# Kernel tuning notes

Measured on AMD Instinct MI355X. Metric: run time of the kernel, lower is better.

Reference implementation:

```python
import jax, jax.numpy as jnp
import numpy as np

E = 512
H = 8
HD = E // H  # head dim = 64


def setup_inputs() -> dict:
    key = jax.random.key(0)
    ks = jax.random.split(key, 7)
    B, P, R = 32, 4096, 64
    visual_tokens = jax.random.normal(ks[0], (B, P, E), dtype=jnp.float32)
    region_tokens = jax.random.normal(ks[1], (B, R, E), dtype=jnp.float32)
    distance_mask = jax.random.uniform(ks[2], (B, P, R), dtype=jnp.float32)
    s = 1.0 / np.sqrt(E)
    in_proj_weight = jax.random.uniform(ks[3], (3 * E, E), jnp.float32, -s, s)
    in_proj_bias = jnp.zeros((3 * E,), jnp.float32)
    out_proj_weight = jax.random.uniform(ks[4], (E, E), jnp.float32, -s, s)
    out_proj_bias = jnp.zeros((E,), jnp.float32)
    return {
        "visual_tokens": visual_tokens,
        "region_tokens": region_tokens,
        "distance_mask": distance_mask,
        "in_proj_weight": in_proj_weight,
        "in_proj_bias": in_proj_bias,
        "out_proj_weight": out_proj_weight,
        "out_proj_bias": out_proj_bias,
    }


def reference(visual_tokens, region_tokens, distance_mask,
              in_proj_weight, in_proj_bias, out_proj_weight, out_proj_bias):
    B, P, _ = visual_tokens.shape
    R = region_tokens.shape[1]
    # additive logit bias derived from distance mask (broadcast over heads,
    # instead of repeating B*H copies like the torch code)
    bias = (1.0 - distance_mask.astype(jnp.float32)) * -1e9  # [B,P,R]
    Wq, Wk, Wv = in_proj_weight[:E], in_proj_weight[E:2 * E], in_proj_weight[2 * E:]
    bq, bk, bv = in_proj_bias[:E], in_proj_bias[E:2 * E], in_proj_bias[2 * E:]
    v32 = visual_tokens.astype(jnp.float32)
    r32 = region_tokens.astype(jnp.float32)
    q = (v32 @ Wq.T + bq).reshape(B, P, H, HD)
    k = (r32 @ Wk.T + bk).reshape(B, R, H, HD)
    v = (r32 @ Wv.T + bv).reshape(B, R, H, HD)
    scale = 1.0 / jnp.sqrt(jnp.float32(HD))
    scores = jnp.einsum('bphd,brhd->bhpr', q, k) * scale + bias[:, None]  # [B,H,P,R]
    attn = jax.nn.softmax(scores, axis=-1)
    ctx = jnp.einsum('bhpr,brhd->bphd', attn, v).reshape(B, P, E)
    attended = ctx @ out_proj_weight.T + out_proj_bias
    return attended.astype(visual_tokens.dtype) + visual_tokens
```

## Files before the change

### kernel.cpp

```cpp
#include <hip/hip_runtime.h>
#include <hip/hip_bf16.h>

typedef unsigned short u16;
typedef unsigned int u32;

using bf16x8 = __attribute__((ext_vector_type(8))) short;
using f32x4  = __attribute__((ext_vector_type(4))) float;

#define MFMA16(a, b, c) __builtin_amdgcn_mfma_f32_16x16x32_bf16((a), (b), (c), 0, 0, 0)

__device__ __forceinline__ u16 f2bf(float f) {
    u32 u = __builtin_bit_cast(u32, f);
    u = (u + 0x7fffu + ((u >> 16) & 1u)) >> 16;
    return (u16)u;
}

__global__ __launch_bounds__(256, 2) void frgca_prep(
    const float* __restrict__ region,
    const float* __restrict__ in_w,
    const float* __restrict__ in_b,
    const float* __restrict__ out_w,
    u16* __restrict__ wq, u16* __restrict__ wo,
    u16* __restrict__ kt, u16* __restrict__ vt)
{
    __shared__ u16 As2[64 * 520];
    const int tid = threadIdx.x;
    const int bid = blockIdx.x;

    if (bid < 32) {
        const float4* w4q = (const float4*)in_w;
        const float4* w4o = (const float4*)out_w;
        int t = bid * 256 + tid;
#pragma unroll
        for (int i = 0; i < 16; ++i) {
            int idx = t + i * 8192;
            float4 v;
            u16* dst;
            if (idx < 65536) { v = w4q[idx]; dst = wq + idx * 4; }
            else             { v = w4o[idx - 65536]; dst = wo + (idx - 65536) * 4; }
            ushort4 o;
            o.x = f2bf(v.x); o.y = f2bf(v.y); o.z = f2bf(v.z); o.w = f2bf(v.w);
            *(ushort4*)dst = o;
        }
        return;
    }

    const int t2 = bid - 32;
    const int b  = t2 >> 2;
    const int nc = t2 & 3;

    {
        const float4* r4 = (const float4*)(region + (size_t)b * 64 * 512);
#pragma unroll
        for (int i = 0; i < 32; ++i) {
            int f4  = tid + i * 256;
            int row = f4 >> 7;
            int c4  = f4 & 127;
            float4 v = r4[f4];
            ushort4 o;
            o.x = f2bf(v.x); o.y = f2bf(v.y); o.z = f2bf(v.z); o.w = f2bf(v.w);
            *(ushort4*)&As2[row * 520 + c4 * 4] = o;
        }
    }
    __syncthreads();

    const int lane = tid & 63, w = tid >> 6;
    const int lo16 = lane & 15, g = lane >> 4;
    const int e0 = nc * 256 + w * 64;

    f32x4 acc[4][4];
#pragma unroll
    for (int mt = 0; mt < 4; ++mt)
#pragma unroll
        for (int nt = 0; nt < 4; ++nt)
            acc[mt][nt] = f32x4{0.f, 0.f, 0.f, 0.f};

    const float* w2 = in_w + 512 * 512;

#pragma unroll 2
    for (int ks = 0; ks < 16; ++ks) {
        const int kc = ks * 32 + 8 * g;
        bf16x8 a[4], bb[4];
#pragma unroll
        for (int mt = 0; mt < 4; ++mt)
            a[mt] = *(const bf16x8*)&As2[(mt * 16 + lo16) * 520 + kc];
#pragma unroll
        for (int nt = 0; nt < 4; ++nt) {
            const int e = e0 + nt * 16 + lo16;
            const float* src = w2 + (size_t)e * 512 + kc;
            float4 v0 = *(const float4*)src;
            float4 v1 = *(const float4*)(src + 4);
            bf16x8 bv;
            bv[0] = (short)f2bf(v0.x); bv[1] = (short)f2bf(v0.y);
            bv[2] = (short)f2bf(v0.z); bv[3] = (short)f2bf(v0.w);
            bv[4] = (short)f2bf(v1.x); bv[5] = (short)f2bf(v1.y);
            bv[6] = (short)f2bf(v1.z); bv[7] = (short)f2bf(v1.w);
            bb[nt] = bv;
        }
#pragma unroll
        for (int mt = 0; mt < 4; ++mt)
#pragma unroll
            for (int nt = 0; nt < 4; ++nt)
                acc[mt][nt] = MFMA16(a[mt], bb[nt], acc[mt][nt]);
    }

#pragma unroll
    for (int nt = 0; nt < 4; ++nt) {
        const int e = e0 + nt * 16 + lo16;
        const float bias = in_b[512 + e];
#pragma unroll
        for (int mt = 0; mt < 4; ++mt)
#pragma unroll
            for (int i = 0; i < 4; ++i) {
                const int r = mt * 16 + 4 * g + i;
                const u16 o = f2bf(acc[mt][nt][i] + bias);
                if (e < 512) {
                    const int h = e >> 6, d = e & 63;
                    kt[(((size_t)(b * 8 + h)) * 64 + r) * 64 + d] = o;
                } else {
                    const int e2 = e - 512;
                    const int h = e2 >> 6, d = e2 & 63;
                    vt[(((size_t)(b * 8 + h)) * 64 + d) * 64 + r] = o;
                }
            }
    }
}

__global__ __launch_bounds__(512, 2) void frgca_main(
    const float* __restrict__ visual,
    const float* __restrict__ mask,
    const float* __restrict__ in_b,
    const float* __restrict__ out_b,
    const u16* __restrict__ wq, const u16* __restrict__ wo,
    const u16* __restrict__ kt, const u16* __restrict__ vt,
    float* __restrict__ out)
{
    __shared__ char regA[73728];
    __shared__ float Ms[64][65];

    const int tid = threadIdx.x;
    const int w = tid >> 6, lane = tid & 63;
    const int lo16 = lane & 15, g = lane >> 4;
    const int pt = blockIdx.x, b = blockIdx.y;
    const int P0 = pt * 64;
    const size_t vbase = ((size_t)(b * 4096 + P0)) * 512;

    u16* As = (u16*)regA;

    {
        const float4* v4 = (const float4*)(visual + vbase);
#pragma unroll
        for (int i = 0; i < 16; ++i) {
            int f4  = tid + i * 512;
            int row = f4 >> 7, c4 = f4 & 127;
            float4 v = v4[f4];
            ushort4 o;
            o.x = f2bf(v.x); o.y = f2bf(v.y); o.z = f2bf(v.z); o.w = f2bf(v.w);
            *(ushort4*)&As[row * 520 + c4 * 4] = o;
        }
        const float4* m4 = (const float4*)(mask + ((size_t)(b * 4096 + P0)) * 64);
#pragma unroll
        for (int i = 0; i < 2; ++i) {
            int f4  = tid + i * 512;
            int row = f4 >> 4, c4 = f4 & 15;
            float4 v = m4[f4];
            float* dst = &Ms[row][c4 * 4];
            dst[0] = (1.0f - v.x) * -1e9f;
            dst[1] = (1.0f - v.y) * -1e9f;
            dst[2] = (1.0f - v.z) * -1e9f;
            dst[3] = (1.0f - v.w) * -1e9f;
        }
    }
    __syncthreads();

    const int e0 = w * 64;

    f32x4 acc[4][4];
#pragma unroll
    for (int mt = 0; mt < 4; ++mt)
#pragma unroll
        for (int nt = 0; nt < 4; ++nt)
            acc[mt][nt] = f32x4{0.f, 0.f, 0.f, 0.f};

#pragma unroll 2
    for (int ks = 0; ks < 16; ++ks) {
        const int kc = ks * 32 + 8 * g;
        bf16x8 a[4], bb[4];
#pragma unroll
        for (int mt = 0; mt < 4; ++mt)
            a[mt] = *(const bf16x8*)&As[(mt * 16 + lo16) * 520 + kc];
#pragma unroll
        for (int nt = 0; nt < 4; ++nt)
            bb[nt] = *(const bf16x8*)&wq[((size_t)(e0 + nt * 16 + lo16)) * 512 + kc];
#pragma unroll
        for (int mt = 0; mt < 4; ++mt)
#pragma unroll
            for (int nt = 0; nt < 4; ++nt)
                acc[mt][nt] = MFMA16(a[mt], bb[nt], acc[mt][nt]);
    }
#pragma unroll
    for (int nt = 0; nt < 4; ++nt) {
        const float bq = in_b[e0 + nt * 16 + lo16];
#pragma unroll
        for (int mt = 0; mt < 4; ++mt)
#pragma unroll
            for (int i = 0; i < 4; ++i)
                acc[mt][nt][i] += bq;
    }
    __syncthreads();

    u16* Qw = (u16*)(regA + w * 9216);
#pragma unroll
    for (int mt = 0; mt < 4; ++mt)
#pragma unroll
        for (int nt = 0; nt < 4; ++nt)
#pragma unroll
            for (int i = 0; i < 4; ++i)
                Qw[(mt * 16 + 4 * g + i) * 72 + (nt * 16 + lo16)] = f2bf(acc[mt][nt][i]);

    const u16* KtH = kt + ((size_t)(b * 8 + w)) * 64 * 64;
    f32x4 s[4][4];
#pragma unroll
    for (int mt = 0; mt < 4; ++mt)
#pragma unroll
        for (int nt = 0; nt < 4; ++nt)
            s[mt][nt] = f32x4{0.f, 0.f, 0.f, 0.f};

#pragma unroll
    for (int ks = 0; ks < 2; ++ks) {
        const int kc = ks * 32 + 8 * g;
        bf16x8 ak[4], bq_[4];
#pragma unroll
        for (int mt = 0; mt < 4; ++mt)
            ak[mt] = *(const bf16x8*)&KtH[(mt * 16 + lo16) * 64 + kc];
#pragma unroll
        for (int nt = 0; nt < 4; ++nt)
            bq_[nt] = *(const bf16x8*)&Qw[(nt * 16 + lo16) * 72 + kc];
#pragma unroll
        for (int mt = 0; mt < 4; ++mt)
#pragma unroll
            for (int nt = 0; nt < 4; ++nt)
                s[mt][nt] = MFMA16(ak[mt], bq_[nt], s[mt][nt]);
    }

#pragma unroll
    for (int nt = 0; nt < 4; ++nt) {
        const int p = nt * 16 + lo16;
        float mx = -3.4e38f;
#pragma unroll
        for (int mt = 0; mt < 4; ++mt)
#pragma unroll
            for (int i = 0; i < 4; ++i) {
                float v = s[mt][nt][i] * 0.125f + Ms[p][mt * 16 + 4 * g + i];
                s[mt][nt][i] = v;
                mx = fmaxf(mx, v);
            }
        mx = fmaxf(mx, __shfl_xor(mx, 16));
        mx = fmaxf(mx, __shfl_xor(mx, 32));
        float sum = 0.f;
#pragma unroll
        for (int mt = 0; mt < 4; ++mt)
#pragma unroll
            for (int i = 0; i < 4; ++i) {
                float ev = __expf(s[mt][nt][i] - mx);
                s[mt][nt][i] = ev;
                sum += ev;
            }
        sum += __shfl_xor(sum, 16);
        sum += __shfl_xor(sum, 32);
        const float inv = 1.0f / sum;
#pragma unroll
        for (int mt = 0; mt < 4; ++mt)
#pragma unroll
            for (int i = 0; i < 4; ++i)
                Qw[p * 72 + (mt * 16 + 4 * g + i)] = f2bf(s[mt][nt][i] * inv);
    }

    const u16* VtH = vt + ((size_t)(b * 8 + w)) * 64 * 64;
    f32x4 c_[4][4];
#pragma unroll
    for (int mt = 0; mt < 4; ++mt)
#pragma unroll
        for (int nt = 0; nt < 4; ++nt)
            c_[mt][nt] = f32x4{0.f, 0.f, 0.f, 0.f};

#pragma unroll
    for (int ks = 0; ks < 2; ++ks) {
        const int kc = ks * 32 + 8 * g;
        bf16x8 av[4], bs_[4];
#pragma unroll
        for (int mt = 0; mt < 4; ++mt)
            av[mt] = *(const bf16x8*)&VtH[(mt * 16 + lo16) * 64 + kc];
#pragma unroll
        for (int nt = 0; nt < 4; ++nt)
            bs_[nt] = *(const bf16x8*)&Qw[(nt * 16 + lo16) * 72 + kc];
#pragma unroll
        for (int mt = 0; mt < 4; ++mt)
#pragma unroll
            for (int nt = 0; nt < 4; ++nt)
                c_[mt][nt] = MFMA16(av[mt], bs_[nt], c_[mt][nt]);
    }
    __syncthreads();

    u16* Cs = (u16*)regA;
#pragma unroll
    for (int mt = 0; mt < 4; ++mt)
#pragma unroll
        for (int nt = 0; nt < 4; ++nt)
#pragma unroll
            for (int i = 0; i < 4; ++i) {
                const int d = mt * 16 + 4 * g + i;
                const int p = nt * 16 + lo16;
                Cs[p * 520 + (w * 64 + d)] = f2bf(c_[mt][nt][i]);
            }
    __syncthreads();

    f32x4 o_[4][4];
#pragma unroll
    for (int mt = 0; mt < 4; ++mt)
#pragma unroll
        for (int nt = 0; nt < 4; ++nt)
            o_[mt][nt] = f32x4{0.f, 0.f, 0.f, 0.f};

#pragma unroll 2
    for (int ks = 0; ks < 16; ++ks) {
        const int kc = ks * 32 + 8 * g;
        bf16x8 a[4], bb[4];
#pragma unroll
        for (int mt = 0; mt < 4; ++mt)
            a[mt] = *(const bf16x8*)&Cs[(mt * 16 + lo16) * 520 + kc];
#pragma unroll
        for (int nt = 0; nt < 4; ++nt)
            bb[nt] = *(const bf16x8*)&wo[((size_t)(e0 + nt * 16 + lo16)) * 512 + kc];
#pragma unroll
        for (int mt = 0; mt < 4; ++mt)
#pragma unroll
            for (int nt = 0; nt < 4; ++nt)
                o_[mt][nt] = MFMA16(a[mt], bb[nt], o_[mt][nt]);
    }

#pragma unroll
    for (int nt = 0; nt < 4; ++nt) {
        const int e = e0 + nt * 16 + lo16;
        const float bo = out_b[e];
#pragma unroll
        for (int mt = 0; mt < 4; ++mt)
#pragma unroll
            for (int i = 0; i < 4; ++i) {
                const int p = mt * 16 + 4 * g + i;
                const size_t gid = vbase + (size_t)p * 512 + e;
                out[gid] = o_[mt][nt][i] + bo + visual[gid];
            }
    }
}

extern "C" void kernel_launch(void* const* d_in, const int* in_sizes, int n_in,
                              void* d_out, int out_size, void* d_ws, size_t ws_size,
                              hipStream_t stream) {
    const float* visual = (const float*)d_in[0];
    const float* region = (const float*)d_in[1];
    const float* mask   = (const float*)d_in[2];
    const float* in_w   = (const float*)d_in[3];
    const float* in_b   = (const float*)d_in[4];
    const float* out_w  = (const float*)d_in[5];
    const float* out_b  = (const float*)d_in[6];
    float* out = (float*)d_out;

    char* ws = (char*)d_ws;
    u16* wq = (u16*)(ws + 0);
    u16* wo = (u16*)(ws + 524288);
    u16* kt = (u16*)(ws + 1048576);
    u16* vt = (u16*)(ws + 3145728);

    frgca_prep<<<dim3(160), dim3(256), 0, stream>>>(region, in_w, in_b, out_w, wq, wo, kt, vt);
    frgca_main<<<dim3(64, 32), dim3(512), 0, stream>>>(visual, mask, in_b, out_b, wq, wo, kt, vt, out);
}
```

Baseline: 478.1 us.

## Swizzle LDS layouts, prefetch weights, and raise occupancy of fused attention kernel

Replaces padded shared-memory tiles with XOR-swizzled layouts (1024-byte rows for activations, 128-byte rows per wave for Q/probabilities, XOR-indexed mask), which cuts LDS use from about 90KB to 80KB. Launch bounds change from 2 to 4 blocks, and the weight loads in both projection GEMMs are software-pipelined with register double-buffering. K and V fragments are loaded early so their latency is hidden. The aim is fewer bank conflicts and better latency hiding, at the cost of register pressure under the tighter occupancy bound. LDS size may still limit residency below the new bound.

```diff
diff --git a/kernel.cpp b/kernel.cpp
--- a/kernel.cpp
+++ b/kernel.cpp
@@ -126,7 +126,7 @@
     }
 }
 
-__global__ __launch_bounds__(512, 2) void frgca_main(
+__global__ __launch_bounds__(512, 4) void frgca_main(
     const float* __restrict__ visual,
     const float* __restrict__ mask,
     const float* __restrict__ in_b,
@@ -135,17 +135,16 @@
     const u16* __restrict__ kt, const u16* __restrict__ vt,
     float* __restrict__ out)
 {
-    __shared__ char regA[73728];
-    __shared__ float Ms[64][65];
+    __shared__ char regA[65536];
+    __shared__ float Ms[4096];
 
     const int tid = threadIdx.x;
     const int w = tid >> 6, lane = tid & 63;
     const int lo16 = lane & 15, g = lane >> 4;
+    const int xr = (lo16 & 7) << 4;
     const int pt = blockIdx.x, b = blockIdx.y;
     const int P0 = pt * 64;
     const size_t vbase = ((size_t)(b * 4096 + P0)) * 512;
-
-    u16* As = (u16*)regA;
 
     {
         const float4* v4 = (const float4*)(visual + vbase);
@@ -156,19 +155,19 @@
             float4 v = v4[f4];
             ushort4 o;
             o.x = f2bf(v.x); o.y = f2bf(v.y); o.z = f2bf(v.z); o.w = f2bf(v.w);
-            *(ushort4*)&As[row * 520 + c4 * 4] = o;
+            *(ushort4*)(regA + row * 1024 + ((c4 * 8) ^ ((row & 7) << 4))) = o;
         }
         const float4* m4 = (const float4*)(mask + ((size_t)(b * 4096 + P0)) * 64);
 #pragma unroll
         for (int i = 0; i < 2; ++i) {
-            int f4  = tid + i * 512;
-            int row = f4 >> 4, c4 = f4 & 15;
+            int f4 = tid + i * 512;
+            int p = f4 >> 4, r0 = (f4 & 15) * 4;
             float4 v = m4[f4];
-            float* dst = &Ms[row][c4 * 4];
-            dst[0] = (1.0f - v.x) * -1e9f;
-            dst[1] = (1.0f - v.y) * -1e9f;
-            dst[2] = (1.0f - v.z) * -1e9f;
-            dst[3] = (1.0f - v.w) * -1e9f;
+            int pb = p * 64, px = p & 31;
+            Ms[pb + ((r0 + 0) ^ px)] = (1.0f - v.x) * -1e9f;
+            Ms[pb + ((r0 + 1) ^ px)] = (1.0f - v.y) * -1e9f;
+            Ms[pb + ((r0 + 2) ^ px)] = (1.0f - v.z) * -1e9f;
+            Ms[pb + ((r0 + 3) ^ px)] = (1.0f - v.w) * -1e9f;
         }
     }
     __syncthreads();
@@ -182,22 +181,56 @@
         for (int nt = 0; nt < 4; ++nt)
             acc[mt][nt] = f32x4{0.f, 0.f, 0.f, 0.f};
 
-#pragma unroll 2
+    const u16* wqR0 = wq + ((size_t)(e0 + 0 * 16 + lo16)) * 512;
+    const u16* wqR1 = wq + ((size_t)(e0 + 1 * 16 + lo16)) * 512;
+    const u16* wqR2 = wq + ((size_t)(e0 + 2 * 16 + lo16)) * 512;
+    const u16* wqR3 = wq + ((size_t)(e0 + 3 * 16 + lo16)) * 512;
+    bf16x8 nb0 = *(const bf16x8*)&wqR0[8 * g];
+    bf16x8 nb1 = *(const bf16x8*)&wqR1[8 * g];
+    bf16x8 nb2 = *(const bf16x8*)&wqR2[8 * g];
+    bf16x8 nb3 = *(const bf16x8*)&wqR3[8 * g];
+
+#pragma unroll
     for (int ks = 0; ks < 16; ++ks) {
         const int kc = ks * 32 + 8 * g;
-        bf16x8 a[4], bb[4];
-#pragma unroll
-        for (int mt = 0; mt < 4; ++mt)
-            a[mt] = *(const bf16x8*)&As[(mt * 16 + lo16) * 520 + kc];
-#pragma unroll
-        for (int nt = 0; nt < 4; ++nt)
-            bb[nt] = *(const bf16x8*)&wq[((size_t)(e0 + nt * 16 + lo16)) * 512 + kc];
-#pragma unroll
-        for (int mt = 0; mt < 4; ++mt)
-#pragma unroll
-            for (int nt = 0; nt < 4; ++nt)
-                acc[mt][nt] = MFMA16(a[mt], bb[nt], acc[mt][nt]);
-    }
+        bf16x8 cb0 = nb0, cb1 = nb1, cb2 = nb2, cb3 = nb3;
+        if (ks < 15) {
+            const int kn = kc + 32;
+            nb0 = *(const bf16x8*)&wqR0[kn];
+            nb1 = *(const bf16x8*)&wqR1[kn];
+            nb2 = *(const bf16x8*)&wqR2[kn];
+            nb3 = *(const bf16x8*)&wqR3[kn];
+        }
+        bf16x8 a[4];
+#pragma unroll
+        for (int mt = 0; mt < 4; ++mt)
+            a[mt] = *(const bf16x8*)(regA + (mt * 16 + lo16) * 1024 + ((kc * 2) ^ xr));
+        acc[0][0] = MFMA16(a[0], cb0, acc[0][0]);
+        acc[1][0] = MFMA16(a[1], cb0, acc[1][0]);
+        acc[2][0] = MFMA16(a[2], cb0, acc[2][0]);
+        acc[3][0] = MFMA16(a[3], cb0, acc[3][0]);
+        acc[0][1] = MFMA16(a[0], cb1, acc[0][1]);
+        acc[1][1] = MFMA16(a[1], cb1, acc[1][1]);
+        acc[2][1] = MFMA16(a[2], cb1, acc[2][1]);
+        acc[3][1] = MFMA16(a[3], cb1, acc[3][1]);
+        acc[0][2] = MFMA16(a[0], cb2, acc[0][2]);
+        acc[1][2] = MFMA16(a[1], cb2, acc[1][2]);
+        acc[2][2] = MFMA16(a[2], cb2, acc[2][2]);
+        acc[3][2] = MFMA16(a[3], cb2, acc[3][2]);
+        acc[0][3] = MFMA16(a[0], cb3, acc[0][3]);
+        acc[1][3] = MFMA16(a[1], cb3, acc[1][3]);
+        acc[2][3] = MFMA16(a[2], cb3, acc[2][3]);
+        acc[3][3] = MFMA16(a[3], cb3, acc[3][3]);
+    }
+
+    const u16* KtH = kt + ((size_t)(b * 8 + w)) * 4096;
+    bf16x8 ak[4][2];
+#pragma unroll
+    for (int ks2 = 0; ks2 < 2; ++ks2)
+#pragma unroll
+        for (int mt = 0; mt < 4; ++mt)
+            ak[mt][ks2] = *(const bf16x8*)&KtH[(mt * 16 + lo16) * 64 + ks2 * 32 + 8 * g];
+
 #pragma unroll
     for (int nt = 0; nt < 4; ++nt) {
         const float bq = in_b[e0 + nt * 16 + lo16];
@@ -209,16 +242,18 @@
     }
     __syncthreads();
 
-    u16* Qw = (u16*)(regA + w * 9216);
-#pragma unroll
-    for (int mt = 0; mt < 4; ++mt)
-#pragma unroll
-        for (int nt = 0; nt < 4; ++nt)
-#pragma unroll
-            for (int i = 0; i < 4; ++i)
-                Qw[(mt * 16 + 4 * g + i) * 72 + (nt * 16 + lo16)] = f2bf(acc[mt][nt][i]);
-
-    const u16* KtH = kt + ((size_t)(b * 8 + w)) * 64 * 64;
+    char* Qw = regA + w * 8192;
+#pragma unroll
+    for (int mt = 0; mt < 4; ++mt)
+#pragma unroll
+        for (int nt = 0; nt < 4; ++nt)
+#pragma unroll
+            for (int i = 0; i < 4; ++i) {
+                const int p = mt * 16 + 4 * g + i;
+                const int d = nt * 16 + lo16;
+                *(u16*)(Qw + p * 128 + ((d * 2) ^ ((p & 7) << 4))) = f2bf(acc[mt][nt][i]);
+            }
+
     f32x4 s[4][4];
 #pragma unroll
     for (int mt = 0; mt < 4; ++mt)
@@ -227,31 +262,37 @@
             s[mt][nt] = f32x4{0.f, 0.f, 0.f, 0.f};
 
 #pragma unroll
-    for (int ks = 0; ks < 2; ++ks) {
-        const int kc = ks * 32 + 8 * g;
-        bf16x8 ak[4], bq_[4];
-#pragma unroll
-        for (int mt = 0; mt < 4; ++mt)
-            ak[mt] = *(const bf16x8*)&KtH[(mt * 16 + lo16) * 64 + kc];
-#pragma unroll
-        for (int nt = 0; nt < 4; ++nt)
-            bq_[nt] = *(const bf16x8*)&Qw[(nt * 16 + lo16) * 72 + kc];
+    for (int ks2 = 0; ks2 < 2; ++ks2) {
+        const int kcb = (ks2 * 32 + 8 * g) * 2;
+        bf16x8 bq_[4];
+#pragma unroll
+        for (int nt = 0; nt < 4; ++nt)
+            bq_[nt] = *(const bf16x8*)(Qw + (nt * 16 + lo16) * 128 + (kcb ^ xr));
 #pragma unroll
         for (int mt = 0; mt < 4; ++mt)
 #pragma unroll
             for (int nt = 0; nt < 4; ++nt)
-                s[mt][nt] = MFMA16(ak[mt], bq_[nt], s[mt][nt]);
-    }
+                s[mt][nt] = MFMA16(ak[mt][ks2], bq_[nt], s[mt][nt]);
+    }
+
+    const u16* VtH = vt + ((size_t)(b * 8 + w)) * 4096;
+    bf16x8 av[4][2];
+#pragma unroll
+    for (int ks2 = 0; ks2 < 2; ++ks2)
+#pragma unroll
+        for (int mt = 0; mt < 4; ++mt)
+            av[mt][ks2] = *(const bf16x8*)&VtH[(mt * 16 + lo16) * 64 + ks2 * 32 + 8 * g];
 
 #pragma unroll
     for (int nt = 0; nt < 4; ++nt) {
         const int p = nt * 16 + lo16;
+        const int pb = p * 64, px = p & 31;
         float mx = -3.4e38f;
 #pragma unroll
         for (int mt = 0; mt < 4; ++mt)
 #pragma unroll
             for (int i = 0; i < 4; ++i) {
-                float v = s[mt][nt][i] * 0.125f + Ms[p][mt * 16 + 4 * g + i];
+                float v = s[mt][nt][i] * 0.125f + Ms[pb + ((mt * 16 + 4 * g + i) ^ px)];
                 s[mt][nt][i] = v;
                 mx = fmaxf(mx, v);
             }
@@ -272,11 +313,12 @@
 #pragma unroll
         for (int mt = 0; mt < 4; ++mt)
 #pragma unroll
-            for (int i = 0; i < 4; ++i)
-                Qw[p * 72 + (mt * 16 + 4 * g + i)] = f2bf(s[mt][nt][i] * inv);
-    }
-
-    const u16* VtH = vt + ((size_t)(b * 8 + w)) * 64 * 64;
+            for (int i = 0; i < 4; ++i) {
+                const int r = mt * 16 + 4 * g + i;
+                *(u16*)(Qw + p * 128 + ((r * 2) ^ ((p & 7) << 4))) = f2bf(s[mt][nt][i] * inv);
+            }
+    }
+
     f32x4 c_[4][4];
 #pragma unroll
     for (int mt = 0; mt < 4; ++mt)
@@ -285,33 +327,29 @@
             c_[mt][nt] = f32x4{0.f, 0.f, 0.f, 0.f};
 
 #pragma unroll
-    for (int ks = 0; ks < 2; ++ks) {
-        const int kc = ks * 32 + 8 * g;
-        bf16x8 av[4], bs_[4];
-#pragma unroll
-        for (int mt = 0; mt < 4; ++mt)
-            av[mt] = *(const bf16x8*)&VtH[(mt * 16 + lo16) * 64 + kc];
-#pragma unroll
-        for (int nt = 0; nt < 4; ++nt)
-            bs_[nt] = *(const bf16x8*)&Qw[(nt * 16 + lo16) * 72 + kc];
+    for (int ks2 = 0; ks2 < 2; ++ks2) {
+        const int kcb = (ks2 * 32 + 8 * g) * 2;
+        bf16x8 bs_[4];
+#pragma unroll
+        for (int nt = 0; nt < 4; ++nt)
+            bs_[nt] = *(const bf16x8*)(Qw + (nt * 16 + lo16) * 128 + (kcb ^ xr));
 #pragma unroll
         for (int mt = 0; mt < 4; ++mt)
 #pragma unroll
             for (int nt = 0; nt < 4; ++nt)
-                c_[mt][nt] = MFMA16(av[mt], bs_[nt], c_[mt][nt]);
+                c_[mt][nt] = MFMA16(av[mt][ks2], bs_[nt], c_[mt][nt]);
     }
     __syncthreads();
 
-    u16* Cs = (u16*)regA;
-#pragma unroll
-    for (int mt = 0; mt < 4; ++mt)
-#pragma unroll
-        for (int nt = 0; nt < 4; ++nt)
-#pragma unroll
-            for (int i = 0; i < 4; ++i) {
-                const int d = mt * 16 + 4 * g + i;
+#pragma unroll
+    for (int mt = 0; mt < 4; ++mt)
+#pragma unroll
+        for (int nt = 0; nt < 4; ++nt)
+#pragma unroll
+            for (int i = 0; i < 4; ++i) {
                 const int p = nt * 16 + lo16;
-                Cs[p * 520 + (w * 64 + d)] = f2bf(c_[mt][nt][i]);
+                const int c = e0 + mt * 16 + 4 * g + i;
+                *(u16*)(regA + p * 1024 + ((c * 2) ^ ((p & 7) << 4))) = f2bf(c_[mt][nt][i]);
             }
     __syncthreads();
 
@@ -322,21 +360,46 @@
         for (int nt = 0; nt < 4; ++nt)
             o_[mt][nt] = f32x4{0.f, 0.f, 0.f, 0.f};
 
-#pragma unroll 2
+    const u16* woR0 = wo + ((size_t)(e0 + 0 * 16 + lo16)) * 512;
+    const u16* woR1 = wo + ((size_t)(e0 + 1 * 16 + lo16)) * 512;
+    const u16* woR2 = wo + ((size_t)(e0 + 2 * 16 + lo16)) * 512;
+    const u16* woR3 = wo + ((size_t)(e0 + 3 * 16 + lo16)) * 512;
+    bf16x8 ob0 = *(const bf16x8*)&woR0[8 * g];
+    bf16x8 ob1 = *(const bf16x8*)&woR1[8 * g];
+    bf16x8 ob2 = *(const bf16x8*)&woR2[8 * g];
+    bf16x8 ob3 = *(const bf16x8*)&woR3[8 * g];
+
+#pragma unroll
     for (int ks = 0; ks < 16; ++ks) {
         const int kc = ks * 32 + 8 * g;
-        bf16x8 a[4], bb[4];
-#pragma unroll
-        for (int mt = 0; mt < 4; ++mt)
-            a[mt] = *(const bf16x8*)&Cs[(mt * 16 + lo16) * 520 + kc];
-#pragma unroll
-        for (int nt = 0; nt < 4; ++nt)
-            bb[nt] = *(const bf16x8*)&wo[((size_t)(e0 + nt * 16 + lo16)) * 512 + kc];
-#pragma unroll
-        for (int mt = 0; mt < 4; ++mt)
-#pragma unroll
-            for (int nt = 0; nt < 4; ++nt)
-                o_[mt][nt] = MFMA16(a[mt], bb[nt], o_[mt][nt]);
+        bf16x8 cb0 = ob0, cb1 = ob1, cb2 = ob2, cb3 = ob3;
+        if (ks < 15) {
+            const int kn = kc + 32;
+            ob0 = *(const bf16x8*)&woR0[kn];
+            ob1 = *(const bf16x8*)&woR1[kn];
+            ob2 = *(const bf16x8*)&woR2[kn];
+            ob3 = *(const bf16x8*)&woR3[kn];
+        }
+        bf16x8 a[4];
+#pragma unroll
+        for (int mt = 0; mt < 4; ++mt)
+            a[mt] = *(const bf16x8*)(regA + (mt * 16 + lo16) * 1024 + ((kc * 2) ^ xr));
+        o_[0][0] = MFMA16(a[0], cb0, o_[0][0]);
+        o_[1][0] = MFMA16(a[1], cb0, o_[1][0]);
+        o_[2][0] = MFMA16(a[2], cb0, o_[2][0]);
+        o_[3][0] = MFMA16(a[3], cb0, o_[3][0]);
+        o_[0][1] = MFMA16(a[0], cb1, o_[0][1]);
+        o_[1][1] = MFMA16(a[1], cb1, o_[1][1]);
+        o_[2][1] = MFMA16(a[2], cb1, o_[2][1]);
+        o_[3][1] = MFMA16(a[3], cb1, o_[3][1]);
+        o_[0][2] = MFMA16(a[0], cb2, o_[0][2]);
+        o_[1][2] = MFMA16(a[1], cb2, o_[1][2]);
+        o_[2][2] = MFMA16(a[2], cb2, o_[2][2]);
+        o_[3][2] = MFMA16(a[3], cb2, o_[3][2]);
+        o_[0][3] = MFMA16(a[0], cb3, o_[0][3]);
+        o_[1][3] = MFMA16(a[1], cb3, o_[1][3]);
+        o_[2][3] = MFMA16(a[2], cb3, o_[2][3]);
+        o_[3][3] = MFMA16(a[3], cb3, o_[3][3]);
     }
 
 #pragma unroll
```

Result: no change. 483.2 us (+1.1%).
